# Optimization experiments

Hardware: AMD Instinct MI355X
Metric: run time of the kernel (lower is better)

Reference implementation:

```python
import jax, jax.numpy as jnp
import numpy as np


def setup_inputs() -> dict:
    key = jax.random.key(0)
    N, E, H, V, C, D, L = 10000, 50000, 128, 8, 5, 59, 2
    keys = iter(jax.random.split(key, 64))

    def p(*shape):
        return jax.random.normal(next(keys), shape, jnp.float32) * 0.05

    inp = dict(
        edge_index=jax.random.randint(next(keys), (2, E), 0, N),
        edge_attr=jax.random.normal(next(keys), (E, D), jnp.float32),
        delta_t=jnp.array([60.0], jnp.float32),
        memory=jnp.ones((N, H), jnp.float32),
        # edge_embed
        W_ee=p(H, D), b_ee=p(H),
        # edge_weight_gen
        W_ewg=p(V, 2 * H), b_ewg=p(V),
        # multi-view GIN convs (L layers, shared MLP across views)
        gin_W1=p(L, H, H), gin_b1=p(L, H), gin_W2=p(L, H, H), gin_b2=p(L, H),
        # Bochner time encoder
        W_t=p(H, 1), b_t=p(H),
        # GRUCell (torch gate order r,z,n)
        W_ih=p(3 * H, H), b_ih=p(3 * H), W_hh=p(3 * H, H), b_hh=p(3 * H),
        # update_nn (feeds detached memory only; not in returned outputs)
        W_up=p(H, V * H), b_up=p(H),
        # local attention (kdim=vdim=2H, 1 head)
        Wq_l=p(H, H), bq_l=p(H), Wk_l=p(H, 2 * H), bk_l=p(H),
        Wv_l=p(H, 2 * H), bv_l=p(H), Wo_l=p(H, H), bo_l=p(H),
        # global attention (1 head)
        Wq_g=p(H, H), bq_g=p(H), Wk_g=p(H, H), bk_g=p(H),
        Wv_g=p(H, H), bv_g=p(H), Wo_g=p(H, H), bo_g=p(H),
        # classifier MLP
        Wc1=p(H, 3 * H), bc1=p(H), Wc2=p(C, H), bc2=p(C),
    )
    return inp


def reference(edge_index, edge_attr, delta_t, memory,
              W_ee, b_ee, W_ewg, b_ewg,
              gin_W1, gin_b1, gin_W2, gin_b2,
              W_t, b_t, W_ih, b_ih, W_hh, b_hh, W_up, b_up,
              Wq_l, bq_l, Wk_l, bk_l, Wv_l, bv_l, Wo_l, bo_l,
              Wq_g, bq_g, Wk_g, bk_g, Wv_g, bv_g, Wo_g, bo_g,
              Wc1, bc1, Wc2, bc2):
    relu = jax.nn.relu
    N, H = memory.shape
    V = W_ewg.shape[0]
    L = gin_W1.shape[0]

    # ---- snapshot encoder (MultiGraphLayer) ----
    ea = relu(edge_attr @ W_ee.T + b_ee)                               # [E,H]
    src0, dst0 = edge_index[0], edge_index[1]
    ew = jax.nn.sigmoid(
        jnp.concatenate([ea, memory[src0]], -1) @ W_ewg.T + b_ewg)     # [E,V]
    h = jnp.broadcast_to(memory[:, None, :], (N, V, H))                # [N,V,H]
    cs, cd = dst0, src0  # edge_index flipped before convs (edge_index[[1,0]])
    for l in range(L):
        # multi-view GIN: view-weighted message + residual MLP update
        msg = relu(h[cs] + ea[:, None, :]) * ew[:, :, None]            # [E,V,H]
        agg = jax.ops.segment_sum(msg, cd, num_segments=N)             # [N,V,H]
        upd = relu((h + agg) @ gin_W1[l].T + gin_b1[l]) @ gin_W2[l].T + gin_b2[l]
        h = h + upd
    h_before = h

    # ---- GRU memory update (vectorized over the V 'class' slots) ----
    te = jnp.sin(delta_t[:, None] * W_t[:, 0] + b_t)                   # [1,H]
    x_in = h + te                                                      # [N,V,H]
    gi = x_in @ W_ih.T + b_ih                                          # [N,V,3H]
    gh = (memory @ W_hh.T + b_hh)[:, None, :]                          # [N,1,3H]
    r = jax.nn.sigmoid(gi[..., :H] + gh[..., :H])
    z = jax.nn.sigmoid(gi[..., H:2 * H] + gh[..., H:2 * H])
    n = jnp.tanh(gi[..., 2 * H:] + r * gh[..., 2 * H:])
    h_new = (1.0 - z) * n + z * memory[:, None, :]                     # [N,V,H]

    # ---- global/local attention fusion ----
    scale = 1.0 / jnp.sqrt(jnp.asarray(H, jnp.float32))
    sf, df = h_new[src0], h_new[dst0]                                  # [E,V,H]
    Wk1, Wk2 = Wk_l[:, :H], Wk_l[:, H:]  # split cat([src,dst]) projection
    Wv1, Wv2 = Wv_l[:, :H], Wv_l[:, H:]
    q_l = ea @ Wq_l.T + bq_l                                           # [E,H]
    K_l = sf @ Wk1.T + df @ Wk2.T + bk_l                               # [E,V,H]
    V_l = sf @ Wv1.T + df @ Wv2.T + bv_l
    a_l = jax.nn.softmax(jnp.einsum('eh,evh->ev', q_l, K_l) * scale, -1)
    local_out = jnp.einsum('ev,evh->eh', a_l, V_l) @ Wo_l.T + bo_l     # [E,H]

    pooled = h_new.mean(axis=0)                                        # [V,H]
    q_g = ea @ Wq_g.T + bq_g
    K_g = pooled @ Wk_g.T + bk_g
    V_g = pooled @ Wv_g.T + bv_g
    a_g = jax.nn.softmax((q_g @ K_g.T) * scale, axis=-1)               # [E,V]
    global_out = (a_g @ V_g) @ Wo_g.T + bo_g                           # [E,H]

    combined = jnp.concatenate([ea, local_out, global_out], axis=-1)   # [E,3H]
    logits = relu(combined @ Wc1.T + bc1) @ Wc2.T + bc2                # [E,C]
    return (logits, ew, h_before, a_g[:, None, :])
```

## Files before the change

kernel.cpp:

```cpp
#include <hip/hip_runtime.h>
#include <cstddef>


#define HSZ 128
typedef unsigned short ushortT;
typedef short short8 __attribute__((ext_vector_type(8)));
typedef float f32x4 __attribute__((ext_vector_type(4)));

__device__ __forceinline__ float sigm(float x) { return 1.f / (1.f + __expf(-x)); }

__device__ __forceinline__ ushortT f2bf(float f) {
  unsigned int u = __float_as_uint(f);
  u += 0x7fffu + ((u >> 16) & 1u);
  return (ushortT)(u >> 16);
}
__device__ __forceinline__ float bf2f(ushortT u) {
  return __uint_as_float(((unsigned int)u) << 16);
}

__device__ __forceinline__ int swzA(int row, int chunk) {
  return row * 64 + (((chunk ^ row) & 7) << 3);
}
__device__ __forceinline__ int swzT(int row, int chunk) {
  return row * 128 + (((chunk & 8) | ((chunk ^ row) & 7)) << 3);
}

template<int ASRC, int ACT, bool OUTBF, bool ABF, bool WBF>
__global__ __launch_bounds__(256) void gemm_bf(
    const void* __restrict__ A1, const void* __restrict__ A2, const void* __restrict__ A3,
    const void* __restrict__ W, const float* __restrict__ bias,
    void* __restrict__ out_, int M, int K, int Nout)
{
  __shared__ short Ash[128 * 64];
  __shared__ short Bsh[128 * 64];
  float* out = (float*)out_;
  ushortT* outh = (ushortT*)out_;
  const int tid = threadIdx.x;
  const int m0 = blockIdx.x * 128;
  const int n0 = blockIdx.y * 128;
  const int l = tid & 63, w = tid >> 6;
  const int wr = w >> 1, wc = w & 1;
  const int lr = l & 15, lq = l >> 4;
  f32x4 acc[4][4] = {};

  for (int k0 = 0; k0 < K; k0 += 64) {
    __syncthreads();
    const bool fast = (k0 + 64 <= K);
    #pragma unroll
    for (int i = 0; i < 4; ++i) {
      int c = i * 256 + tid;
      int row = c >> 3, seg = c & 7;
      int kb = k0 + seg * 8;
      {
        int m = m0 + row;
        short8 pk;
        if (ABF) {
          if (m < M) {
            if (ASRC == 3) {
              const ushortT* S = (kb < 128) ? (const ushortT*)A1
                               : (kb < 256) ? (const ushortT*)A2 : (const ushortT*)A3;
              pk = *reinterpret_cast<const short8*>(S + (size_t)m * 128 + (kb & 127));
            } else {
              pk = *reinterpret_cast<const short8*>((const ushortT*)A1 + (size_t)m * K + kb);
            }
          } else {
            #pragma unroll
            for (int j = 0; j < 8; ++j) pk[j] = 0;
          }
        } else {
          const float* A1f = (const float*)A1;
          float v[8];
          if (fast && m < M) {
            const float4* p = reinterpret_cast<const float4*>(A1f + (size_t)m * K + kb);
            float4 x0 = p[0], x1 = p[1];
            v[0]=x0.x; v[1]=x0.y; v[2]=x0.z; v[3]=x0.w;
            v[4]=x1.x; v[5]=x1.y; v[6]=x1.z; v[7]=x1.w;
          } else {
            #pragma unroll
            for (int j = 0; j < 8; ++j) {
              int k = kb + j;
              v[j] = (m < M && k < K) ? A1f[(size_t)m * K + k] : 0.f;
            }
          }
          #pragma unroll
          for (int j = 0; j < 8; ++j) pk[j] = (short)f2bf(v[j]);
        }
        *reinterpret_cast<short8*>(&Ash[swzA(row, seg)]) = pk;
      }
      {
        int nn = n0 + row;
        short8 pk;
        if (WBF) {
          if (nn < Nout)
            pk = *reinterpret_cast<const short8*>((const ushortT*)W + (size_t)nn * K + kb);
          else {
            #pragma unroll
            for (int j = 0; j < 8; ++j) pk[j] = 0;
          }
        } else {
          const float* Wf = (const float*)W;
          float v[8];
          if (fast && nn < Nout) {
            const float4* p = reinterpret_cast<const float4*>(Wf + (size_t)nn * K + kb);
            float4 x0 = p[0], x1 = p[1];
            v[0]=x0.x; v[1]=x0.y; v[2]=x0.z; v[3]=x0.w;
            v[4]=x1.x; v[5]=x1.y; v[6]=x1.z; v[7]=x1.w;
          } else {
            #pragma unroll
            for (int j = 0; j < 8; ++j) {
              int k = kb + j;
              v[j] = (nn < Nout && k < K) ? Wf[(size_t)nn * K + k] : 0.f;
            }
          }
          #pragma unroll
          for (int j = 0; j < 8; ++j) pk[j] = (short)f2bf(v[j]);
        }
        *reinterpret_cast<short8*>(&Bsh[swzA(row, seg)]) = pk;
      }
    }
    __syncthreads();
    #pragma unroll
    for (int ks = 0; ks < 2; ++ks) {
      short8 a[4], b[4];
      #pragma unroll
      for (int mi = 0; mi < 4; ++mi)
        a[mi] = *reinterpret_cast<const short8*>(&Ash[swzA(wr*64 + mi*16 + lr, ks*4 + lq)]);
      #pragma unroll
      for (int ni = 0; ni < 4; ++ni)
        b[ni] = *reinterpret_cast<const short8*>(&Bsh[swzA(wc*64 + ni*16 + lr, ks*4 + lq)]);
      #pragma unroll
      for (int mi = 0; mi < 4; ++mi)
        #pragma unroll
        for (int ni = 0; ni < 4; ++ni)
          acc[mi][ni] = __builtin_amdgcn_mfma_f32_16x16x32_bf16(a[mi], b[ni], acc[mi][ni], 0, 0, 0);
    }
  }
  #pragma unroll
  for (int ni = 0; ni < 4; ++ni) {
    int col = n0 + wc*64 + ni*16 + lr;
    if (col >= Nout) continue;
    float bz = bias ? bias[col] : 0.f;
    #pragma unroll
    for (int mi = 0; mi < 4; ++mi) {
      int mb = m0 + wr*64 + mi*16 + lq*4;
      #pragma unroll
      for (int r = 0; r < 4; ++r) {
        int m = mb + r;
        if (m >= M) continue;
        float vv = acc[mi][ni][r] + bz;
        if (ACT == 1) vv = fmaxf(vv, 0.f);
        size_t o = (size_t)m * Nout + col;
        if (OUTBF) outh[o] = f2bf(vv); else out[o] = vv;
      }
    }
  }
}

template<int LMODE>
__global__ __launch_bounds__(256) void k_gin(
    const ushortT* __restrict__ hb, const ushortT* __restrict__ aggb,
    const float* __restrict__ memf,
    float* __restrict__ houtf, ushortT* __restrict__ houtb,
    const ushortT* __restrict__ W1b, const float* __restrict__ b1,
    const ushortT* __restrict__ W2b, const float* __restrict__ b2, int M)
{
  __shared__ short smem[24576];
  short* Ash  = smem;
  short* Bsh  = smem + 8192;
  short* Tsh  = smem;
  short* B2sh = smem + 16384;
  const int tid = threadIdx.x;
  const int m0 = blockIdx.x * 128;
  const int l = tid & 63, w = tid >> 6;
  const int wr = w >> 1, wc = w & 1;
  const int lr = l & 15, lq = l >> 4;
  f32x4 acc[4][4] = {};

  for (int ks2 = 0; ks2 < 2; ++ks2) {
    if (ks2) __syncthreads();
    #pragma unroll
    for (int i = 0; i < 4; ++i) {
      int c = i * 256 + tid;
      int row = c >> 3, seg = c & 7;
      int kb = ks2 * 64 + seg * 8;
      {
        int m = m0 + row;
        short8 pk;
        if (m < M) {
          short8 hv;
          if (LMODE == 1) hv = *reinterpret_cast<const short8*>(hb + ((size_t)(m >> 3)) * 128 + kb);
          else            hv = *reinterpret_cast<const short8*>(hb + (size_t)m * 128 + kb);
          short8 av = *reinterpret_cast<const short8*>(aggb + (size_t)m * 128 + kb);
          #pragma unroll
          for (int j = 0; j < 8; ++j)
            pk[j] = (short)f2bf(bf2f((ushortT)hv[j]) + bf2f((ushortT)av[j]));
        } else {
          #pragma unroll
          for (int j = 0; j < 8; ++j) pk[j] = 0;
        }
        *reinterpret_cast<short8*>(&Ash[swzA(row, seg)]) = pk;
      }
      *reinterpret_cast<short8*>(&Bsh[swzA(row, seg)]) =
          *reinterpret_cast<const short8*>(W1b + (size_t)row * 128 + kb);
      if (ks2 == 0)
        *reinterpret_cast<short8*>(&B2sh[swzA(row, seg)]) =
            *reinterpret_cast<const short8*>(W2b + (size_t)row * 128 + seg * 8);
    }
    __syncthreads();
    #pragma unroll
    for (int ks = 0; ks < 2; ++ks) {
      short8 a[4], b[4];
      #pragma unroll
      for (int mi = 0; mi < 4; ++mi)
        a[mi] = *reinterpret_cast<const short8*>(&Ash[swzA(wr*64 + mi*16 + lr, ks*4 + lq)]);
      #pragma unroll
      for (int ni = 0; ni < 4; ++ni)
        b[ni] = *reinterpret_cast<const short8*>(&Bsh[swzA(wc*64 + ni*16 + lr, ks*4 + lq)]);
      #pragma unroll
      for (int mi = 0; mi < 4; ++mi)
        #pragma unroll
        for (int ni = 0; ni < 4; ++ni)
          acc[mi][ni] = __builtin_amdgcn_mfma_f32_16x16x32_bf16(a[mi], b[ni], acc[mi][ni], 0, 0, 0);
    }
  }
  __syncthreads();
  {
    float b1v[4];
    #pragma unroll
    for (int ni = 0; ni < 4; ++ni) b1v[ni] = b1[wc*64 + ni*16 + lr];
    #pragma unroll
    for (int mi = 0; mi < 4; ++mi)
      #pragma unroll
      for (int ni = 0; ni < 4; ++ni) {
        int col = wc*64 + ni*16 + lr;
        #pragma unroll
        for (int r = 0; r < 4; ++r) {
          int row = wr*64 + mi*16 + lq*4 + r;
          float v = fmaxf(acc[mi][ni][r] + b1v[ni], 0.f);
          Tsh[swzT(row, col >> 3) + (col & 7)] = (short)f2bf(v);
        }
      }
  }
  __syncthreads();
  f32x4 acc2[4][4] = {};
  for (int ks2 = 0; ks2 < 2; ++ks2) {
    if (ks2) {
      __syncthreads();
      #pragma unroll
      for (int i = 0; i < 4; ++i) {
        int c = i * 256 + tid;
        int row = c >> 3, seg = c & 7;
        *reinterpret_cast<short8*>(&B2sh[swzA(row, seg)]) =
            *reinterpret_cast<const short8*>(W2b + (size_t)row * 128 + 64 + seg * 8);
      }
      __syncthreads();
    }
    #pragma unroll
    for (int ks = 0; ks < 2; ++ks) {
      short8 a[4], b[4];
      #pragma unroll
      for (int mi = 0; mi < 4; ++mi)
        a[mi] = *reinterpret_cast<const short8*>(&Tsh[swzT(wr*64 + mi*16 + lr, ks2*8 + ks*4 + lq)]);
      #pragma unroll
      for (int ni = 0; ni < 4; ++ni)
        b[ni] = *reinterpret_cast<const short8*>(&B2sh[swzA(wc*64 + ni*16 + lr, ks*4 + lq)]);
      #pragma unroll
      for (int mi = 0; mi < 4; ++mi)
        #pragma unroll
        for (int ni = 0; ni < 4; ++ni)
          acc2[mi][ni] = __builtin_amdgcn_mfma_f32_16x16x32_bf16(a[mi], b[ni], acc2[mi][ni], 0, 0, 0);
    }
  }
  {
    float b2v[4];
    #pragma unroll
    for (int ni = 0; ni < 4; ++ni) b2v[ni] = b2[wc*64 + ni*16 + lr];
    #pragma unroll
    for (int ni = 0; ni < 4; ++ni) {
      int col = wc*64 + ni*16 + lr;
      #pragma unroll
      for (int mi = 0; mi < 4; ++mi) {
        int mb = m0 + wr*64 + mi*16 + lq*4;
        #pragma unroll
        for (int r = 0; r < 4; ++r) {
          int m = mb + r;
          if (m >= M) continue;
          float base = (LMODE == 1) ? memf[((size_t)(m >> 3)) * 128 + col]
                                    : bf2f(hb[(size_t)m * 128 + col]);
          float ho = base + acc2[mi][ni][r] + b2v[ni];
          if (LMODE == 1) houtb[(size_t)m * 128 + col] = f2bf(ho);
          else            houtf[(size_t)m * 128 + col] = ho;
        }
      }
    }
  }
}

__global__ __launch_bounds__(512) void k_giru(
    const float* __restrict__ hf, const float* __restrict__ te,
    const ushortT* __restrict__ Wihb, const float* __restrict__ b_ih,
    const float* __restrict__ gh, const float* __restrict__ memory,
    ushortT* __restrict__ hnb, int M)
{
  __shared__ short Ash[8192];
  __shared__ short Bsh[24576];
  const int tid = threadIdx.x;
  const int m0 = blockIdx.x * 64;
  const int l = tid & 63, w = tid >> 6;
  const int lr = l & 15, lq = l >> 4;
  const int r0 = (w >> 1) * 16, c0 = (w & 1) * 64;
  f32x4 acc[3][4] = {};

  #pragma unroll
  for (int i = 0; i < 2; ++i) {
    int c = i * 512 + tid;
    int row = c >> 4, seg = c & 15;
    int m = m0 + row;
    short8 pk;
    if (m < M) {
      const float4* p = reinterpret_cast<const float4*>(hf + (size_t)m * 128 + seg * 8);
      const float4* t = reinterpret_cast<const float4*>(te + seg * 8);
      float4 x0 = p[0], x1 = p[1], t0 = t[0], t1 = t[1];
      pk[0]=(short)f2bf(x0.x+t0.x); pk[1]=(short)f2bf(x0.y+t0.y);
      pk[2]=(short)f2bf(x0.z+t0.z); pk[3]=(short)f2bf(x0.w+t0.w);
      pk[4]=(short)f2bf(x1.x+t1.x); pk[5]=(short)f2bf(x1.y+t1.y);
      pk[6]=(short)f2bf(x1.z+t1.z); pk[7]=(short)f2bf(x1.w+t1.w);
    } else {
      #pragma unroll
      for (int j = 0; j < 8; ++j) pk[j] = 0;
    }
    *reinterpret_cast<short8*>(&Ash[swzT(row, seg)]) = pk;
  }
  for (int ks2 = 0; ks2 < 2; ++ks2) {
    if (ks2) __syncthreads();
    #pragma unroll
    for (int i = 0; i < 6; ++i) {
      int c = i * 512 + tid;
      int row = c >> 3, seg = c & 7;
      *reinterpret_cast<short8*>(&Bsh[swzA(row, seg)]) =
          *reinterpret_cast<const short8*>(Wihb + (size_t)row * 128 + ks2 * 64 + seg * 8);
    }
    __syncthreads();
    #pragma unroll
    for (int ks = 0; ks < 2; ++ks) {
      short8 a = *reinterpret_cast<const short8*>(&Ash[swzT(r0 + lr, ks2*8 + ks*4 + lq)]);
      #pragma unroll
      for (int s = 0; s < 3; ++s)
        #pragma unroll
        for (int xi = 0; xi < 4; ++xi) {
          short8 b = *reinterpret_cast<const short8*>(
              &Bsh[swzA(s*128 + c0 + xi*16 + lr, ks*4 + lq)]);
          acc[s][xi] = __builtin_amdgcn_mfma_f32_16x16x32_bf16(a, b, acc[s][xi], 0, 0, 0);
        }
    }
  }
  #pragma unroll
  for (int xi = 0; xi < 4; ++xi) {
    int x = c0 + xi * 16 + lr;
    float br = b_ih[x], bz = b_ih[128 + x], bn = b_ih[256 + x];
    #pragma unroll
    for (int rr = 0; rr < 4; ++rr) {
      int m = m0 + r0 + lq * 4 + rr;
      if (m >= M) continue;
      int node = m >> 3;
      float ghr = gh[(size_t)node * 384 + x];
      float ghz = gh[(size_t)node * 384 + 128 + x];
      float ghn = gh[(size_t)node * 384 + 256 + x];
      float mem = memory[(size_t)node * 128 + x];
      float rv = sigm(acc[0][xi][rr] + br + ghr);
      float zv = sigm(acc[1][xi][rr] + bz + ghz);
      float nv = tanhf(acc[2][xi][rr] + bn + rv * ghn);
      hnb[(size_t)m * 128 + x] = f2bf((1.f - zv) * nv + zv * mem);
    }
  }
}

__global__ void k_hist(const int* __restrict__ srcI, int* __restrict__ cnt, int E)
{
  int e = blockIdx.x * 256 + threadIdx.x;
  if (e < E) atomicAdd(&cnt[srcI[e]], 1);
}

__global__ __launch_bounds__(1024) void k_scan(const int* __restrict__ cnt,
    int* __restrict__ ofs, int* __restrict__ cur, int N)
{
  __shared__ int buf[1024];
  __shared__ int carry;
  int tid = threadIdx.x;
  if (tid == 0) carry = 0;
  __syncthreads();
  for (int base = 0; base < N; base += 1024) {
    int i = base + tid;
    int v = (i < N) ? cnt[i] : 0;
    buf[tid] = v;
    __syncthreads();
    for (int off = 1; off < 1024; off <<= 1) {
      int t = (tid >= off) ? buf[tid - off] : 0;
      __syncthreads();
      buf[tid] += t;
      __syncthreads();
    }
    int excl = carry + buf[tid] - v;
    if (i < N) { ofs[i] = excl; cur[i] = excl; }
    __syncthreads();
    if (tid == 0) carry += buf[1023];
    __syncthreads();
  }
  if (tid == 0) ofs[N] = carry;
}

__global__ void k_fill(const int* __restrict__ srcI, int* __restrict__ cur,
                       int* __restrict__ eid, int E)
{
  int e = blockIdx.x * 256 + threadIdx.x;
  if (e >= E) return;
  int p = atomicAdd(&cur[srcI[e]], 1);
  eid[p] = e;
}

template<int LMODE>
__global__ __launch_bounds__(256) void k_agg(const ushortT* __restrict__ hb,
    const ushortT* __restrict__ eab, const float* __restrict__ ew,
    const int* __restrict__ dstI, const int* __restrict__ ofs,
    const int* __restrict__ eid, ushortT* __restrict__ aggb, int N)
{
  int half = threadIdx.x >> 7;
  int x = threadIdx.x & 127;
  int n = blockIdx.x * 2 + half;
  if (n >= N) return;
  float acc[8] = {};
  int beg = ofs[n], end = ofs[n + 1];
  for (int i = beg; i < end; ++i) {
    int e = eid[i];
    int d = dstI[e];
    float eav = bf2f(eab[(size_t)e * 128 + x]);
    const float* ewp = ew + (size_t)e * 8;
    if (LMODE == 1) {
      float m = fmaxf(bf2f(hb[(size_t)d * 128 + x]) + eav, 0.f);
      #pragma unroll
      for (int v = 0; v < 8; ++v) acc[v] += m * ewp[v];
    } else {
      const ushortT* hd = hb + (size_t)d * 1024;
      #pragma unroll
      for (int v = 0; v < 8; ++v)
        acc[v] += fmaxf(bf2f(hd[v * 128 + x]) + eav, 0.f) * ewp[v];
    }
  }
  ushortT* ag = aggb + (size_t)n * 1024;
  #pragma unroll
  for (int v = 0; v < 8; ++v) ag[v * 128 + x] = f2bf(acc[v]);
}

__global__ __launch_bounds__(256) void k_ew(const ushortT* __restrict__ eab,
    const ushortT* __restrict__ memb, const int* __restrict__ srcI,
    const float* __restrict__ W_ewg, const float* __restrict__ b_ewg,
    float* __restrict__ ew, int E)
{
  __shared__ float Wsh[2048];
  __shared__ float bsh[8];
  int tid = threadIdx.x;
  for (int i = tid; i < 2048; i += 256) Wsh[i] = W_ewg[i];
  if (tid < 8) bsh[tid] = b_ewg[tid];
  __syncthreads();
  int wv = tid >> 6, lane = tid & 63;
  int e = blockIdx.x * 4 + wv;
  if (e >= E) return;
  int s = srcI[e];
  float c0 = bf2f(eab[(size_t)e * 128 + lane]);
  float c1 = bf2f(eab[(size_t)e * 128 + 64 + lane]);
  float c2 = bf2f(memb[(size_t)s * 128 + lane]);
  float c3 = bf2f(memb[(size_t)s * 128 + 64 + lane]);
  #pragma unroll
  for (int v = 0; v < 8; ++v) {
    float p = c0 * Wsh[v * 256 + lane] + c1 * Wsh[v * 256 + 64 + lane]
            + c2 * Wsh[v * 256 + 128 + lane] + c3 * Wsh[v * 256 + 192 + lane];
    #pragma unroll
    for (int o = 32; o; o >>= 1) p += __shfl_down(p, o);
    if (lane == 0) ew[(size_t)e * 8 + v] = sigm(p + bsh[v]);
  }
}

__global__ void k_cvt(const float* __restrict__ src, ushortT* __restrict__ dst, int total)
{
  int i = blockIdx.x * 256 + threadIdx.x;
  if (i < total) dst[i] = f2bf(src[i]);
}

__global__ void k_te(const float* __restrict__ delta_t, const float* __restrict__ W_t,
                     const float* __restrict__ b_t, float* __restrict__ te)
{
  int t = threadIdx.x;
  if (t < 128) te[t] = sinf(delta_t[0] * W_t[t] + b_t[t]);
}

__global__ __launch_bounds__(256) void k_pool(const ushortT* __restrict__ hnb,
                                              float* __restrict__ prw, int N)
{
  int tid = threadIdx.x;
  float acc[4] = {0.f, 0.f, 0.f, 0.f};
  for (int n = blockIdx.x; n < N; n += gridDim.x) {
    const ushortT* row = hnb + (size_t)n * 1024;
    #pragma unroll
    for (int j = 0; j < 4; ++j) acc[j] += bf2f(row[tid + j * 256]);
  }
  #pragma unroll
  for (int j = 0; j < 4; ++j) atomicAdd(&prw[tid + j * 256], acc[j]);
}

__global__ __launch_bounds__(256) void k_prep(
    const float* __restrict__ Wo_l, const float* __restrict__ Wv_l,
    const float* __restrict__ bv_l, const float* __restrict__ bo_l,
    const float* __restrict__ Wq_l, const float* __restrict__ bq_l,
    const float* __restrict__ Wk_l, const float* __restrict__ Wq_g,
    const float* __restrict__ bq_g,
    ushortT* __restrict__ Wl2b, float* __restrict__ blv,
    ushortT* __restrict__ Wqkgb, float* __restrict__ bqkg)
{
  int idx = blockIdx.x * 256 + threadIdx.x;
  if (idx < 32768) {
    int n = idx >> 8, k = idx & 255;
    float a = 0.f;
    for (int j = 0; j < 128; ++j) a += Wo_l[n * 128 + j] * Wv_l[j * 256 + k];
    Wl2b[idx] = f2bf(a);
  } else if (idx < 65536) {
    int rem = idx - 32768;
    int n = rem >> 7, j = rem & 127;
    float a = 0.f;
    for (int k = 0; k < 128; ++k) a += Wq_l[k * 128 + j] * Wk_l[k * 256 + n];
    Wqkgb[rem] = f2bf(a);
  } else {
    int rem = idx - 65536;
    Wqkgb[32768 + rem] = f2bf(Wq_g[rem]);
  }
  if (blockIdx.x == 0 && threadIdx.x < 128) {
    int n = threadIdx.x;
    float a = bo_l[n];
    for (int j = 0; j < 128; ++j) a += Wo_l[n * 128 + j] * bv_l[j];
    blv[n] = a;
  }
  if (blockIdx.x == 1) {
    int n = threadIdx.x;
    float a = 0.f;
    for (int k = 0; k < 128; ++k) a += bq_l[k] * Wk_l[k * 256 + n];
    bqkg[n] = a;
  }
  if (blockIdx.x == 2 && threadIdx.x < 128) bqkg[256 + threadIdx.x] = bq_g[threadIdx.x];
}

__global__ __launch_bounds__(256) void k_kgg(const float* __restrict__ prw,
    const float* __restrict__ Wk_g, const float* __restrict__ Wv_g, const float* __restrict__ bv_g,
    const float* __restrict__ Wo_g, float* __restrict__ Kg, float* __restrict__ G, int N)
{
  __shared__ float pl[1024];
  __shared__ float vg[1024];
  int tid = threadIdx.x;
  float invN = 1.f / (float)N;
  for (int i = tid; i < 1024; i += 256) pl[i] = prw[i] * invN;
  __syncthreads();
  for (int o = tid; o < 1024; o += 256) {
    int v = o >> 7, x = o & 127;
    float a = 0.f, b = 0.f;
    for (int k = 0; k < 128; ++k) {
      float p = pl[v * 128 + k];
      a += p * Wk_g[(size_t)x * 128 + k];
      b += p * Wv_g[(size_t)x * 128 + k];
    }
    Kg[o] = a;
    vg[o] = b + bv_g[x];
  }
  __syncthreads();
  for (int o = tid; o < 1024; o += 256) {
    int v = o >> 7, x = o & 127;
    float a = 0.f;
    for (int k = 0; k < 128; ++k) a += vg[v * 128 + k] * Wo_g[(size_t)x * 128 + k];
    G[o] = a;
  }
}

__global__ __launch_bounds__(256) void k_local(const ushortT* __restrict__ hnb,
    const ushortT* __restrict__ qkgb,
    const int* __restrict__ srcI, const int* __restrict__ dstI,
    ushortT* __restrict__ wsd, int E)
{
  __shared__ float sf[1024], df[1024], q12[256], sc[8];
  int e = blockIdx.x;
  int tid = threadIdx.x;
  int s = srcI[e], d = dstI[e];
  {
    int c = tid & 127;
    const ushortT* srcp = (tid < 128) ? hnb + (size_t)s * 1024 : hnb + (size_t)d * 1024;
    short8 v = *reinterpret_cast<const short8*>(srcp + c * 8);
    float* dl = (tid < 128) ? sf : df;
    #pragma unroll
    for (int j = 0; j < 8; ++j) dl[c * 8 + j] = bf2f((ushortT)v[j]);
  }
  if (tid < 32) {
    short8 v = *reinterpret_cast<const short8*>(qkgb + (size_t)e * 384 + tid * 8);
    #pragma unroll
    for (int j = 0; j < 8; ++j) q12[tid * 8 + j] = bf2f((ushortT)v[j]);
  }
  __syncthreads();
  int wv = tid >> 6, lane = tid & 63;
  for (int v = wv; v < 8; v += 4) {
    float p = q12[lane] * sf[v * 128 + lane] + q12[64 + lane] * sf[v * 128 + 64 + lane]
            + q12[128 + lane] * df[v * 128 + lane] + q12[192 + lane] * df[v * 128 + 64 + lane];
    #pragma unroll
    for (int o = 32; o; o >>= 1) p += __shfl_down(p, o);
    if (lane == 0) sc[v] = p * 0.08838834764831845f;
  }
  __syncthreads();
  float mx = sc[0];
  #pragma unroll
  for (int v = 1; v < 8; ++v) mx = fmaxf(mx, sc[v]);
  float a[8], sum = 0.f;
  #pragma unroll
  for (int v = 0; v < 8; ++v) { a[v] = __expf(sc[v] - mx); sum += a[v]; }
  float inv = 1.f / sum;
  int x = tid & 127;
  const float* mat = (tid < 128) ? sf : df;
  float accv = 0.f;
  #pragma unroll
  for (int v = 0; v < 8; ++v) accv += a[v] * mat[v * 128 + x];
  wsd[(size_t)e * 256 + (tid < 128 ? x : 128 + x)] = f2bf(accv * inv);
}

__global__ __launch_bounds__(256) void k_global(const ushortT* __restrict__ qkgb,
    const float* __restrict__ Kg, const float* __restrict__ G, const float* __restrict__ bo_g,
    float* __restrict__ ag_out, ushortT* __restrict__ goutb, int E)
{
  __shared__ float Kgs[1024], Gs[1024], bs[128];
  int tid = threadIdx.x;
  for (int i = tid; i < 1024; i += 256) { Kgs[i] = Kg[i]; Gs[i] = G[i]; }
  if (tid < 128) bs[tid] = bo_g[tid];
  __syncthreads();
  int wv = tid >> 6, lane = tid & 63;
  int e = blockIdx.x * 4 + wv;
  if (e >= E) return;
  float qa = bf2f(qkgb[(size_t)e * 384 + 256 + lane]);
  float qb = bf2f(qkgb[(size_t)e * 384 + 320 + lane]);
  float s[8];
  #pragma unroll
  for (int v = 0; v < 8; ++v) {
    float p = qa * Kgs[v * 128 + lane] + qb * Kgs[v * 128 + 64 + lane];
    #pragma unroll
    for (int o = 32; o; o >>= 1) p += __shfl_xor(p, o);
    s[v] = p * 0.08838834764831845f;
  }
  float mx = s[0];
  #pragma unroll
  for (int v = 1; v < 8; ++v) mx = fmaxf(mx, s[v]);
  float sum = 0.f;
  #pragma unroll
  for (int v = 0; v < 8; ++v) { s[v] = __expf(s[v] - mx); sum += s[v]; }
  float inv = 1.f / sum;
  #pragma unroll
  for (int v = 0; v < 8; ++v) s[v] *= inv;
  #pragma unroll
  for (int v = 0; v < 8; ++v) if (lane == v) ag_out[(size_t)e * 8 + v] = s[v];
  float g0 = bs[lane], g1 = bs[64 + lane];
  #pragma unroll
  for (int v = 0; v < 8; ++v) {
    g0 += s[v] * Gs[v * 128 + lane];
    g1 += s[v] * Gs[v * 128 + 64 + lane];
  }
  goutb[(size_t)e * 128 + lane] = f2bf(g0);
  goutb[(size_t)e * 128 + 64 + lane] = f2bf(g1);
}

__global__ __launch_bounds__(256) void k_logits(const ushortT* __restrict__ hid,
    const float* __restrict__ Wc2, const float* __restrict__ bc2,
    float* __restrict__ logits, int E)
{
  __shared__ float Wsh[640];
  __shared__ float bsh[5];
  int tid = threadIdx.x;
  for (int i = tid; i < 640; i += 256) Wsh[i] = Wc2[i];
  if (tid < 5) bsh[tid] = bc2[tid];
  __syncthreads();
  int wv = tid >> 6, lane = tid & 63;
  int e = blockIdx.x * 4 + wv;
  if (e >= E) return;
  float h0 = bf2f(hid[(size_t)e * 128 + lane]), h1 = bf2f(hid[(size_t)e * 128 + 64 + lane]);
  #pragma unroll
  for (int c = 0; c < 5; ++c) {
    float p = h0 * Wsh[c * 128 + lane] + h1 * Wsh[c * 128 + 64 + lane];
    #pragma unroll
    for (int o = 32; o; o >>= 1) p += __shfl_down(p, o);
    if (lane == 0) logits[(size_t)e * 5 + c] = p + bsh[c];
  }
}

extern "C" void kernel_launch(void* const* d_in, const int* in_sizes, int n_in,
                              void* d_out, int out_size, void* d_ws, size_t ws_size,
                              hipStream_t stream)
{
  const int*   edge_index = (const int*)d_in[0];
  const float* edge_attr  = (const float*)d_in[1];
  const float* delta_t    = (const float*)d_in[2];
  const float* memory     = (const float*)d_in[3];
  const float* W_ee  = (const float*)d_in[4];
  const float* b_ee  = (const float*)d_in[5];
  const float* W_ewg = (const float*)d_in[6];
  const float* b_ewg = (const float*)d_in[7];
  const float* gin_W1 = (const float*)d_in[8];
  const float* gin_b1 = (const float*)d_in[9];
  const float* gin_W2 = (const float*)d_in[10];
  const float* gin_b2 = (const float*)d_in[11];
  const float* W_t  = (const float*)d_in[12];
  const float* b_t  = (const float*)d_in[13];
  const float* W_ih = (const float*)d_in[14];
  const float* b_ih = (const float*)d_in[15];
  const float* W_hh = (const float*)d_in[16];
  const float* b_hh = (const float*)d_in[17];
  const float* Wq_l = (const float*)d_in[20];
  const float* bq_l = (const float*)d_in[21];
  const float* Wk_l = (const float*)d_in[22];
  const float* Wv_l = (const float*)d_in[24];
  const float* bv_l = (const float*)d_in[25];
  const float* Wo_l = (const float*)d_in[26];
  const float* bo_l = (const float*)d_in[27];
  const float* Wq_g = (const float*)d_in[28];
  const float* bq_g = (const float*)d_in[29];
  const float* Wk_g = (const float*)d_in[30];
  const float* Wv_g = (const float*)d_in[32];
  const float* bv_g = (const float*)d_in[33];
  const float* Wo_g = (const float*)d_in[34];
  const float* bo_g = (const float*)d_in[35];
  const float* Wc1  = (const float*)d_in[36];
  const float* bc1  = (const float*)d_in[37];
  const float* Wc2  = (const float*)d_in[38];
  const float* bc2  = (const float*)d_in[39];

  const int E = in_sizes[0] / 2;
  const int N = in_sizes[3] / HSZ;
  const int* srcI = edge_index;
  const int* dstI = edge_index + E;

  float* out    = (float*)d_out;
  float* logits = out;
  float* ew     = out + (size_t)E * 5;
  float* h      = out + (size_t)E * 13;
  float* ag_out = out + (size_t)E * 13 + (size_t)N * 1024;

  float* ws = (float*)d_ws;
  size_t off = 0;
  auto alloc = [&](size_t n) { size_t o = off; off += (n + 255) & ~(size_t)255; return o; };
  float* te   = ws + alloc(128);
  float* blv  = ws + alloc(128);
  float* bqkg = ws + alloc(384);
  float* Kg   = ws + alloc(1024);
  float* G    = ws + alloc(1024);
  float* prw  = ws + alloc(1024);
  int* cnt = (int*)(ws + alloc(N));
  int* ofs = (int*)(ws + alloc(N + 1));
  int* cur = (int*)(ws + alloc(N));
  int* eid = (int*)(ws + alloc(E));
  ushortT* memb   = (ushortT*)(ws + alloc((size_t)N * 64));
  ushortT* eab    = (ushortT*)(ws + alloc((size_t)E * 64));
  ushortT* h1b    = (ushortT*)(ws + alloc((size_t)N * 512));
  ushortT* hnb    = (ushortT*)(ws + alloc((size_t)N * 512));
  float*   gh     = ws + alloc((size_t)N * 384);
  ushortT* ginW1b = (ushortT*)(ws + alloc(16384));
  ushortT* ginW2b = (ushortT*)(ws + alloc(16384));
  ushortT* Wihb   = (ushortT*)(ws + alloc(24576));
  ushortT* Wc1b   = (ushortT*)(ws + alloc(24576));
  ushortT* Wl2b   = (ushortT*)(ws + alloc(16384));
  ushortT* Wqkgb  = (ushortT*)(ws + alloc(24576));
  size_t brA = (size_t)N * 512, brC = (size_t)E * 448;
  size_t brsz = brA > brC ? brA : brC;
  float* BR = ws + alloc(brsz);
  if (ws_size < off * sizeof(float)) return;

  ushortT* aggb = (ushortT*)BR;
  ushortT* qkgb = (ushortT*)BR;
  ushortT* wsd  = (ushortT*)(BR + (size_t)E * 192);
  ushortT* lclb = (ushortT*)(BR + (size_t)E * 320);
  ushortT* glbb = (ushortT*)(BR + (size_t)E * 384);
  ushortT* hid  = (ushortT*)BR;

  auto cdiv = [](int a, int b) { return (a + b - 1) / b; };

  hipMemsetAsync(cnt, 0, (size_t)N * sizeof(int), stream);
  k_hist<<<cdiv(E, 256), 256, 0, stream>>>(srcI, cnt, E);
  k_scan<<<1, 1024, 0, stream>>>(cnt, ofs, cur, N);
  k_fill<<<cdiv(E, 256), 256, 0, stream>>>(srcI, cur, eid, E);
  k_cvt<<<cdiv(N * 128, 256), 256, 0, stream>>>(memory, memb, N * 128);
  k_cvt<<<128, 256, 0, stream>>>(gin_W1, ginW1b, 32768);
  k_cvt<<<128, 256, 0, stream>>>(gin_W2, ginW2b, 32768);
  k_cvt<<<192, 256, 0, stream>>>(W_ih, Wihb, 49152);
  k_cvt<<<192, 256, 0, stream>>>(Wc1, Wc1b, 49152);
  gemm_bf<0, 1, true, false, false><<<dim3(cdiv(E, 128), 1), 256, 0, stream>>>(
      edge_attr, nullptr, nullptr, W_ee, b_ee, eab, E, 59, 128);
  k_ew<<<cdiv(E, 4), 256, 0, stream>>>(eab, memb, srcI, W_ewg, b_ewg, ew, E);
  k_te<<<1, 128, 0, stream>>>(delta_t, W_t, b_t, te);
  k_prep<<<320, 256, 0, stream>>>(Wo_l, Wv_l, bv_l, bo_l, Wq_l, bq_l, Wk_l, Wq_g, bq_g,
                                  Wl2b, blv, Wqkgb, bqkg);
  gemm_bf<0, 0, false, false, false><<<dim3(cdiv(N, 128), 3), 256, 0, stream>>>(
      memory, nullptr, nullptr, W_hh, b_hh, gh, N, 128, 384);
  k_agg<1><<<cdiv(N, 2), 256, 0, stream>>>(memb, eab, ew, dstI, ofs, eid, aggb, N);
  k_gin<1><<<cdiv(N * 8, 128), 256, 0, stream>>>(
      memb, aggb, memory, nullptr, h1b, ginW1b, gin_b1, ginW2b, gin_b2, N * 8);
  k_agg<2><<<cdiv(N, 2), 256, 0, stream>>>(h1b, eab, ew, dstI, ofs, eid, aggb, N);
  k_gin<2><<<cdiv(N * 8, 128), 256, 0, stream>>>(
      h1b, aggb, nullptr, h, nullptr, ginW1b + 16384, gin_b1 + 128,
      ginW2b + 16384, gin_b2 + 128, N * 8);
  k_giru<<<cdiv(N * 8, 64), 512, 0, stream>>>(h, te, Wihb, b_ih, gh, memory, hnb, N * 8);
  hipMemsetAsync(prw, 0, 1024 * sizeof(float), stream);
  k_pool<<<256, 256, 0, stream>>>(hnb, prw, N);
  k_kgg<<<1, 256, 0, stream>>>(prw, Wk_g, Wv_g, bv_g, Wo_g, Kg, G, N);
  gemm_bf<0, 0, true, true, true><<<dim3(cdiv(E, 128), 3), 256, 0, stream>>>(
      eab, nullptr, nullptr, Wqkgb, bqkg, qkgb, E, 128, 384);
  k_local<<<E, 256, 0, stream>>>(hnb, qkgb, srcI, dstI, wsd, E);
  gemm_bf<0, 0, true, true, true><<<dim3(cdiv(E, 128), 1), 256, 0, stream>>>(
      wsd, nullptr, nullptr, Wl2b, blv, lclb, E, 256, 128);
  k_global<<<cdiv(E, 4), 256, 0, stream>>>(qkgb, Kg, G, bo_g, ag_out, glbb, E);
  gemm_bf<3, 1, true, true, true><<<dim3(cdiv(E, 128), 1), 256, 0, stream>>>(
      eab, lclb, glbb, Wc1b, bc1, hid, E, 384, 128);
  k_logits<<<cdiv(E, 4), 256, 0, stream>>>(hid, Wc2, bc2, logits, E);
}
```

Baseline: 585.5 us.

## Fuse local and global attention into one warp-per-edge kernel; store gh in bf16

Merges the per-edge local attention kernel (one block per edge, staging through shared memory) with the global attention kernel into a single kernel where each wavefront handles one edge in registers, using packed bf16 pair loads and shuffle reductions. Also stores the W_hh GEMM output as bf16 and reads memory from its bf16 copy in the GIN and GRU epilogues, cutting global traffic. The cost is lower precision on gh and memory, and more registers per thread in the fused kernel.

```diff
diff --git a/kernel.cpp b/kernel.cpp
--- a/kernel.cpp
+++ b/kernel.cpp
@@ -4,6 +4,7 @@
 
 #define HSZ 128
 typedef unsigned short ushortT;
+typedef unsigned int uintT;
 typedef short short8 __attribute__((ext_vector_type(8)));
 typedef float f32x4 __attribute__((ext_vector_type(4)));
 
@@ -16,6 +17,11 @@
 }
 __device__ __forceinline__ float bf2f(ushortT u) {
   return __uint_as_float(((unsigned int)u) << 16);
+}
+__device__ __forceinline__ float bflo(uintT u) { return __uint_as_float(u << 16); }
+__device__ __forceinline__ float bfhi(uintT u) { return __uint_as_float(u & 0xffff0000u); }
+__device__ __forceinline__ uintT pk2bf(float a, float b) {
+  return ((uintT)f2bf(b) << 16) | (uintT)f2bf(a);
 }
 
 __device__ __forceinline__ int swzA(int row, int chunk) {
@@ -159,7 +165,6 @@
 template<int LMODE>
 __global__ __launch_bounds__(256) void k_gin(
     const ushortT* __restrict__ hb, const ushortT* __restrict__ aggb,
-    const float* __restrict__ memf,
     float* __restrict__ houtf, ushortT* __restrict__ houtb,
     const ushortT* __restrict__ W1b, const float* __restrict__ b1,
     const ushortT* __restrict__ W2b, const float* __restrict__ b2, int M)
@@ -285,7 +290,7 @@
         for (int r = 0; r < 4; ++r) {
           int m = mb + r;
           if (m >= M) continue;
-          float base = (LMODE == 1) ? memf[((size_t)(m >> 3)) * 128 + col]
+          float base = (LMODE == 1) ? bf2f(hb[((size_t)(m >> 3)) * 128 + col])
                                     : bf2f(hb[(size_t)m * 128 + col]);
           float ho = base + acc2[mi][ni][r] + b2v[ni];
           if (LMODE == 1) houtb[(size_t)m * 128 + col] = f2bf(ho);
@@ -299,7 +304,7 @@
 __global__ __launch_bounds__(512) void k_giru(
     const float* __restrict__ hf, const float* __restrict__ te,
     const ushortT* __restrict__ Wihb, const float* __restrict__ b_ih,
-    const float* __restrict__ gh, const float* __restrict__ memory,
+    const ushortT* __restrict__ ghb, const ushortT* __restrict__ memb,
     ushortT* __restrict__ hnb, int M)
 {
   __shared__ short Ash[8192];
@@ -363,10 +368,10 @@
       int m = m0 + r0 + lq * 4 + rr;
       if (m >= M) continue;
       int node = m >> 3;
-      float ghr = gh[(size_t)node * 384 + x];
-      float ghz = gh[(size_t)node * 384 + 128 + x];
-      float ghn = gh[(size_t)node * 384 + 256 + x];
-      float mem = memory[(size_t)node * 128 + x];
+      float ghr = bf2f(ghb[(size_t)node * 384 + x]);
+      float ghz = bf2f(ghb[(size_t)node * 384 + 128 + x]);
+      float ghn = bf2f(ghb[(size_t)node * 384 + 256 + x]);
+      float mem = bf2f(memb[(size_t)node * 128 + x]);
       float rv = sigm(acc[0][xi][rr] + br + ghr);
       float zv = sigm(acc[1][xi][rr] + bz + ghz);
       float nv = tanhf(acc[2][xi][rr] + bn + rv * ghn);
@@ -577,94 +582,83 @@
   }
 }
 
-__global__ __launch_bounds__(256) void k_local(const ushortT* __restrict__ hnb,
-    const ushortT* __restrict__ qkgb,
+__global__ __launch_bounds__(256) void k_lg(
+    const ushortT* __restrict__ hnb, const ushortT* __restrict__ qkgb,
     const int* __restrict__ srcI, const int* __restrict__ dstI,
-    ushortT* __restrict__ wsd, int E)
-{
-  __shared__ float sf[1024], df[1024], q12[256], sc[8];
-  int e = blockIdx.x;
-  int tid = threadIdx.x;
-  int s = srcI[e], d = dstI[e];
-  {
-    int c = tid & 127;
-    const ushortT* srcp = (tid < 128) ? hnb + (size_t)s * 1024 : hnb + (size_t)d * 1024;
-    short8 v = *reinterpret_cast<const short8*>(srcp + c * 8);
-    float* dl = (tid < 128) ? sf : df;
-    #pragma unroll
-    for (int j = 0; j < 8; ++j) dl[c * 8 + j] = bf2f((ushortT)v[j]);
-  }
-  if (tid < 32) {
-    short8 v = *reinterpret_cast<const short8*>(qkgb + (size_t)e * 384 + tid * 8);
-    #pragma unroll
-    for (int j = 0; j < 8; ++j) q12[tid * 8 + j] = bf2f((ushortT)v[j]);
-  }
-  __syncthreads();
-  int wv = tid >> 6, lane = tid & 63;
-  for (int v = wv; v < 8; v += 4) {
-    float p = q12[lane] * sf[v * 128 + lane] + q12[64 + lane] * sf[v * 128 + 64 + lane]
-            + q12[128 + lane] * df[v * 128 + lane] + q12[192 + lane] * df[v * 128 + 64 + lane];
-    #pragma unroll
-    for (int o = 32; o; o >>= 1) p += __shfl_down(p, o);
-    if (lane == 0) sc[v] = p * 0.08838834764831845f;
-  }
-  __syncthreads();
-  float mx = sc[0];
-  #pragma unroll
-  for (int v = 1; v < 8; ++v) mx = fmaxf(mx, sc[v]);
-  float a[8], sum = 0.f;
-  #pragma unroll
-  for (int v = 0; v < 8; ++v) { a[v] = __expf(sc[v] - mx); sum += a[v]; }
-  float inv = 1.f / sum;
-  int x = tid & 127;
-  const float* mat = (tid < 128) ? sf : df;
-  float accv = 0.f;
-  #pragma unroll
-  for (int v = 0; v < 8; ++v) accv += a[v] * mat[v * 128 + x];
-  wsd[(size_t)e * 256 + (tid < 128 ? x : 128 + x)] = f2bf(accv * inv);
-}
-
-__global__ __launch_bounds__(256) void k_global(const ushortT* __restrict__ qkgb,
-    const float* __restrict__ Kg, const float* __restrict__ G, const float* __restrict__ bo_g,
-    float* __restrict__ ag_out, ushortT* __restrict__ goutb, int E)
+    const float* __restrict__ Kg, const float* __restrict__ G,
+    const float* __restrict__ bo_g,
+    float* __restrict__ ag_out, ushortT* __restrict__ wsd,
+    ushortT* __restrict__ glbb, int E)
 {
   __shared__ float Kgs[1024], Gs[1024], bs[128];
   int tid = threadIdx.x;
   for (int i = tid; i < 1024; i += 256) { Kgs[i] = Kg[i]; Gs[i] = G[i]; }
   if (tid < 128) bs[tid] = bo_g[tid];
   __syncthreads();
-  int wv = tid >> 6, lane = tid & 63;
-  int e = blockIdx.x * 4 + wv;
+  int w = tid >> 6, l = tid & 63;
+  int e = blockIdx.x * 4 + w;
   if (e >= E) return;
-  float qa = bf2f(qkgb[(size_t)e * 384 + 256 + lane]);
-  float qb = bf2f(qkgb[(size_t)e * 384 + 320 + lane]);
-  float s[8];
+  int s = srcI[e], d = dstI[e];
+  const uintT* qrow = reinterpret_cast<const uintT*>(qkgb + (size_t)e * 384);
+  const uintT* srow = reinterpret_cast<const uintT*>(hnb + (size_t)s * 1024);
+  const uintT* drow = reinterpret_cast<const uintT*>(hnb + (size_t)d * 1024);
+  uintT q1u = qrow[l], q2u = qrow[64 + l], qgu = qrow[128 + l];
+  float q1a = bflo(q1u), q1b = bfhi(q1u);
+  float q2a = bflo(q2u), q2b = bfhi(q2u);
+  float qga = bflo(qgu), qgb_ = bfhi(qgu);
+  float sfa[8], sfb[8], dfa[8], dfb[8], pl[8], pg[8];
   #pragma unroll
   for (int v = 0; v < 8; ++v) {
-    float p = qa * Kgs[v * 128 + lane] + qb * Kgs[v * 128 + 64 + lane];
-    #pragma unroll
-    for (int o = 32; o; o >>= 1) p += __shfl_xor(p, o);
-    s[v] = p * 0.08838834764831845f;
-  }
-  float mx = s[0];
-  #pragma unroll
-  for (int v = 1; v < 8; ++v) mx = fmaxf(mx, s[v]);
-  float sum = 0.f;
-  #pragma unroll
-  for (int v = 0; v < 8; ++v) { s[v] = __expf(s[v] - mx); sum += s[v]; }
-  float inv = 1.f / sum;
-  #pragma unroll
-  for (int v = 0; v < 8; ++v) s[v] *= inv;
-  #pragma unroll
-  for (int v = 0; v < 8; ++v) if (lane == v) ag_out[(size_t)e * 8 + v] = s[v];
-  float g0 = bs[lane], g1 = bs[64 + lane];
+    uintT su = srow[v * 64 + l], du = drow[v * 64 + l];
+    sfa[v] = bflo(su); sfb[v] = bfhi(su);
+    dfa[v] = bflo(du); dfb[v] = bfhi(du);
+    pl[v] = q1a * sfa[v] + q1b * sfb[v] + q2a * dfa[v] + q2b * dfb[v];
+    float2 kv = *reinterpret_cast<const float2*>(&Kgs[v * 128 + 2 * l]);
+    pg[v] = qga * kv.x + qgb_ * kv.y;
+  }
   #pragma unroll
   for (int v = 0; v < 8; ++v) {
-    g0 += s[v] * Gs[v * 128 + lane];
-    g1 += s[v] * Gs[v * 128 + 64 + lane];
-  }
-  goutb[(size_t)e * 128 + lane] = f2bf(g0);
-  goutb[(size_t)e * 128 + 64 + lane] = f2bf(g1);
+    #pragma unroll
+    for (int m = 1; m <= 32; m <<= 1) {
+      pl[v] += __shfl_xor(pl[v], m);
+      pg[v] += __shfl_xor(pg[v], m);
+    }
+  }
+  const float scale = 0.08838834764831845f;
+  float mx = pl[0];
+  #pragma unroll
+  for (int v = 1; v < 8; ++v) mx = fmaxf(mx, pl[v]);
+  float suml = 0.f, al[8];
+  #pragma unroll
+  for (int v = 0; v < 8; ++v) { al[v] = __expf((pl[v] - mx) * scale); suml += al[v]; }
+  float invl = 1.f / suml;
+  float wsa = 0.f, wsb = 0.f, wda = 0.f, wdb = 0.f;
+  #pragma unroll
+  for (int v = 0; v < 8; ++v) {
+    float a = al[v];
+    wsa += a * sfa[v]; wsb += a * sfb[v];
+    wda += a * dfa[v]; wdb += a * dfb[v];
+  }
+  uintT* wrow = reinterpret_cast<uintT*>(wsd + (size_t)e * 256);
+  wrow[l]      = pk2bf(wsa * invl, wsb * invl);
+  wrow[64 + l] = pk2bf(wda * invl, wdb * invl);
+  float mg = pg[0];
+  #pragma unroll
+  for (int v = 1; v < 8; ++v) mg = fmaxf(mg, pg[v]);
+  float sumg = 0.f, ag[8];
+  #pragma unroll
+  for (int v = 0; v < 8; ++v) { ag[v] = __expf((pg[v] - mg) * scale); sumg += ag[v]; }
+  float invg = 1.f / sumg;
+  if (l < 8) ag_out[(size_t)e * 8 + l] = ag[l] * invg;
+  float2 bv = *reinterpret_cast<const float2*>(&bs[2 * l]);
+  float ga = bv.x, gb = bv.y;
+  #pragma unroll
+  for (int v = 0; v < 8; ++v) {
+    float sv = ag[v] * invg;
+    float2 gv = *reinterpret_cast<const float2*>(&Gs[v * 128 + 2 * l]);
+    ga += sv * gv.x; gb += sv * gv.y;
+  }
+  reinterpret_cast<uintT*>(glbb)[(size_t)e * 64 + l] = pk2bf(ga, gb);
 }
 
 __global__ __launch_bounds__(256) void k_logits(const ushortT* __restrict__ hid,
@@ -759,7 +753,7 @@
   ushortT* eab    = (ushortT*)(ws + alloc((size_t)E * 64));
   ushortT* h1b    = (ushortT*)(ws + alloc((size_t)N * 512));
   ushortT* hnb    = (ushortT*)(ws + alloc((size_t)N * 512));
-  float*   gh     = ws + alloc((size_t)N * 384);
+  ushortT* ghb    = (ushortT*)(ws + alloc((size_t)N * 192));
   ushortT* ginW1b = (ushortT*)(ws + alloc(16384));
   ushortT* ginW2b = (ushortT*)(ws + alloc(16384));
   ushortT* Wihb   = (ushortT*)(ws + alloc(24576));
@@ -795,25 +789,25 @@
   k_te<<<1, 128, 0, stream>>>(delta_t, W_t, b_t, te);
   k_prep<<<320, 256, 0, stream>>>(Wo_l, Wv_l, bv_l, bo_l, Wq_l, bq_l, Wk_l, Wq_g, bq_g,
                                   Wl2b, blv, Wqkgb, bqkg);
-  gemm_bf<0, 0, false, false, false><<<dim3(cdiv(N, 128), 3), 256, 0, stream>>>(
-      memory, nullptr, nullptr, W_hh, b_hh, gh, N, 128, 384);
+  gemm_bf<0, 0, true, false, false><<<dim3(cdiv(N, 128), 3), 256, 0, stream>>>(
+      memory, nullptr, nullptr, W_hh, b_hh, ghb, N, 128, 384);
   k_agg<1><<<cdiv(N, 2), 256, 0, stream>>>(memb, eab, ew, dstI, ofs, eid, aggb, N);
   k_gin<1><<<cdiv(N * 8, 128), 256, 0, stream>>>(
-      memb, aggb, memory, nullptr, h1b, ginW1b, gin_b1, ginW2b, gin_b2, N * 8);
+      memb, aggb, nullptr, h1b, ginW1b, gin_b1, ginW2b, gin_b2, N * 8);
   k_agg<2><<<cdiv(N, 2), 256, 0, stream>>>(h1b, eab, ew, dstI, ofs, eid, aggb, N);
   k_gin<2><<<cdiv(N * 8, 128), 256, 0, stream>>>(
-      h1b, aggb, nullptr, h, nullptr, ginW1b + 16384, gin_b1 + 128,
+      h1b, aggb, h, nullptr, ginW1b + 16384, gin_b1 + 128,
       ginW2b + 16384, gin_b2 + 128, N * 8);
-  k_giru<<<cdiv(N * 8, 64), 512, 0, stream>>>(h, te, Wihb, b_ih, gh, memory, hnb, N * 8);
+  k_giru<<<cdiv(N * 8, 64), 512, 0, stream>>>(h, te, Wihb, b_ih, ghb, memb, hnb, N * 8);
   hipMemsetAsync(prw, 0, 1024 * sizeof(float), stream);
   k_pool<<<256, 256, 0, stream>>>(hnb, prw, N);
   k_kgg<<<1, 256, 0, stream>>>(prw, Wk_g, Wv_g, bv_g, Wo_g, Kg, G, N);
   gemm_bf<0, 0, true, true, true><<<dim3(cdiv(E, 128), 3), 256, 0, stream>>>(
       eab, nullptr, nullptr, Wqkgb, bqkg, qkgb, E, 128, 384);
-  k_local<<<E, 256, 0, stream>>>(hnb, qkgb, srcI, dstI, wsd, E);
+  k_lg<<<cdiv(E, 4), 256, 0, stream>>>(hnb, qkgb, srcI, dstI, Kg, G, bo_g,
+                                       ag_out, wsd, glbb, E);
   gemm_bf<0, 0, true, true, true><<<dim3(cdiv(E, 128), 1), 256, 0, stream>>>(
       wsd, nullptr, nullptr, Wl2b, blv, lclb, E, 256, 128);
-  k_global<<<cdiv(E, 4), 256, 0, stream>>>(qkgb, Kg, G, bo_g, ag_out, glbb, E);
   gemm_bf<3, 1, true, true, true><<<dim3(cdiv(E, 128), 1), 256, 0, stream>>>(
       eab, lclb, glbb, Wc1b, bc1, hid, E, 384, 128);
   k_logits<<<cdiv(E, 4), 256, 0, stream>>>(hid, Wc2, bc2, logits, E);
```

Measured after the change: 542.8 us. 7.3% less time.
